# Kernel optimization log

Hardware: AMD Instinct MI355X
Metric: run time of the kernel (lower is better)

The kernel has to match this reference:

```python
import jax, jax.numpy as jnp
import numpy as np

DIM = 256
N_PATCHES = 2048
N_HEADS = 8
BATCH = 2


def setup_inputs() -> dict:
    key = jax.random.key(0)
    ks = jax.random.split(key, 8)
    d = DIM
    s = d ** -0.5
    return {
        "x": jax.random.normal(ks[0], (BATCH, N_PATCHES, d), dtype=jnp.float32),
        # weights stored (in_features, out_features) so y = x @ W + b
        "W_qk": jax.random.normal(ks[1], (d, 2 * d), dtype=jnp.float32) * s,
        "W_v": jax.random.normal(ks[2], (d, d), dtype=jnp.float32) * s,
        "W_proj": jax.random.normal(ks[3], (d, d), dtype=jnp.float32) * s,
        "b_proj": jnp.zeros((d,), dtype=jnp.float32),
        "W_pos": jax.random.normal(ks[4], (2, N_HEADS), dtype=jnp.float32) * 0.5,
        "b_pos": jnp.zeros((N_HEADS,), dtype=jnp.float32),
        "gating": jnp.ones((N_HEADS,), dtype=jnp.float32),
    }


def reference(x, W_qk, W_v, W_proj, b_proj, W_pos, b_pos, gating):
    B, N, C = x.shape
    H = gating.shape[0]
    Dh = C // H
    scale = Dh ** -0.5

    # content attention: q @ k^T softmax
    qk = (x @ W_qk).reshape(B, N, 2, H, Dh)
    q = jnp.transpose(qk[:, :, 0], (0, 2, 1, 3))  # [B,H,N,Dh]
    k = jnp.transpose(qk[:, :, 1], (0, 2, 1, 3))
    patch_score = jax.nn.softmax(jnp.einsum("bhnd,bhmd->bhnm", q, k) * scale, axis=-1)

    # positional attention from relative indices (d, |d|) -> per-head score
    idx = jnp.arange(N, dtype=jnp.float32)
    rel = idx[:, None] - idx[None, :]                      # [N,N]
    rel_feat = jnp.stack([rel, jnp.abs(rel)], axis=-1)     # [N,N,2]
    pos = rel_feat @ W_pos + b_pos                         # [N,N,H]
    pos_score = jax.nn.softmax(jnp.transpose(pos, (2, 0, 1)), axis=-1)  # [H,N,N]

    g = jax.nn.sigmoid(gating)[None, :, None, None]        # [1,H,1,1]
    attn = (1.0 - g) * patch_score + g * pos_score[None]   # [B,H,N,N]
    attn = attn / jnp.sum(attn, axis=-1, keepdims=True)

    v = jnp.transpose((x @ W_v).reshape(B, N, H, Dh), (0, 2, 1, 3))  # [B,H,N,Dh]
    out = jnp.einsum("bhnm,bhmd->bhnd", attn, v)
    out = jnp.transpose(out, (0, 2, 1, 3)).reshape(B, N, C)
    return out @ W_proj + b_proj
```

## Files before the change

### kernel.cpp

```cpp
#include <hip/hip_runtime.h>
#include <hip/hip_bf16.h>

#define DIM 256
#define NP 2048
#define NH 8
#define BATCH 2
#define DH 32

typedef __attribute__((ext_vector_type(8))) short bshort8;
typedef __attribute__((ext_vector_type(4))) short bshort4;
typedef __attribute__((ext_vector_type(4))) float f32x4;

#define LOG2E 1.44269504f
#define QSCALE (0.17677669529663687f * LOG2E)

union U16B { uint4 u; bshort8 s8; __hip_bfloat16 h[8]; };
union U8B  { uint2 u; bshort4 s4; __hip_bfloat16 h[4]; };

__device__ __forceinline__ float fexp2(float x) { return __builtin_amdgcn_exp2f(x); }
__device__ __forceinline__ unsigned packbf(float hi, float lo) {
    return __builtin_amdgcn_perm(__float_as_uint(hi), __float_as_uint(lo), 0x07060302u);
}

__device__ __forceinline__ int lds_addr(int row, int colg) {
    return row * 256 + (((colg ^ (row & 7)) & 31) << 3);
}

__global__ __launch_bounds__(256) void prep_kernel(
    const float* __restrict__ Wqk,
    const float* __restrict__ Wv,
    const float* __restrict__ Wproj,
    __hip_bfloat16* __restrict__ WT) {
    const int t = threadIdx.x;
    const int blk = blockIdx.x;
    __shared__ float ts[64][65];
    const int ct = blk >> 2, k0 = (blk & 3) * 64;
    const int c0 = ct * 64;
    const float* src; int ldw, cs0; float scl = 1.0f;
    if (ct < 8)       { src = Wqk;   ldw = 512; cs0 = c0;      if (ct < 4) scl = QSCALE; }
    else if (ct < 12) { src = Wv;    ldw = 256; cs0 = c0 - 512; }
    else              { src = Wproj; ldw = 256; cs0 = c0 - 768; }
    const int cc = t & 63, tq = t >> 6;
#pragma unroll
    for (int j = 0; j < 16; j++) {
        int kk = tq * 16 + j;
        ts[kk][cc] = src[(size_t)(k0 + kk) * ldw + cs0 + cc];
    }
    __syncthreads();
    const int kk2 = t & 63;
#pragma unroll
    for (int j = 0; j < 16; j++) {
        int cc2 = tq * 16 + j;
        WT[(size_t)(c0 + cc2) * 256 + k0 + kk2] = __float2bfloat16(ts[kk2][cc2] * scl);
    }
}

__global__ __launch_bounds__(256) void qkv_mfma(
    const float* __restrict__ x,
    const __hip_bfloat16* __restrict__ WT,
    __hip_bfloat16* __restrict__ q,
    __hip_bfloat16* __restrict__ k,
    __hip_bfloat16* __restrict__ vF) {
    __shared__ __align__(16) __hip_bfloat16 As[64 * 256];
    __shared__ __align__(16) __hip_bfloat16 Bs[64 * 256];
    const int t = threadIdx.x, lane = t & 63, wvid = t >> 6;
    const int l15 = lane & 15, l4 = lane >> 4;
    const int m0 = blockIdx.x * 64;
    const int nb0 = blockIdx.y * 64;

#pragma unroll
    for (int j = 0; j < 8; j++) {
        const int flat = j * 2048 + t * 8;
        const int row = flat >> 8, colg = (flat >> 3) & 31;
        float4 f0 = *(const float4*)(x + (size_t)m0 * 256 + flat);
        float4 f1 = *(const float4*)(x + (size_t)m0 * 256 + flat + 4);
        U16B a;
        a.h[0] = __float2bfloat16(f0.x); a.h[1] = __float2bfloat16(f0.y);
        a.h[2] = __float2bfloat16(f0.z); a.h[3] = __float2bfloat16(f0.w);
        a.h[4] = __float2bfloat16(f1.x); a.h[5] = __float2bfloat16(f1.y);
        a.h[6] = __float2bfloat16(f1.z); a.h[7] = __float2bfloat16(f1.w);
        *(uint4*)&As[lds_addr(row, colg)] = a.u;
        *(uint4*)&Bs[lds_addr(row, colg)] = *(const uint4*)(WT + (size_t)nb0 * 256 + flat);
    }
    __syncthreads();

    f32x4 acc[4] = {{0.f,0.f,0.f,0.f},{0.f,0.f,0.f,0.f},{0.f,0.f,0.f,0.f},{0.f,0.f,0.f,0.f}};
#pragma unroll
    for (int kk = 0; kk < 8; kk++) {
        const int colg = kk * 4 + l4;
        U16B bw; bw.u = *(const uint4*)&Bs[lds_addr(wvid * 16 + l15, colg)];
#pragma unroll
        for (int mt = 0; mt < 4; mt++) {
            U16B ax; ax.u = *(const uint4*)&As[lds_addr(mt * 16 + l15, colg)];
            acc[mt] = __builtin_amdgcn_mfma_f32_16x16x32_bf16(ax.s8, bw.s8, acc[mt], 0, 0, 0);
        }
    }

    if (nb0 < 512) {
        __syncthreads();
        __hip_bfloat16* Tr = As;
#pragma unroll
        for (int mt = 0; mt < 4; mt++)
#pragma unroll
            for (int r = 0; r < 4; r++)
                Tr[(mt * 16 + l4 * 4 + r) * 72 + wvid * 16 + l15] = __float2bfloat16(acc[mt][r]);
        __syncthreads();
        const int hh = t >> 7, row = (t >> 1) & 63, part = t & 1;
        const bool isq = (nb0 < 256);
        const int cc = (isq ? nb0 : nb0 - 256) + hh * 32;
        const int hOut = cc >> 5;
        const int tok = m0 + row;
        const int b = tok >> 11, n = tok & (NP - 1);
        __hip_bfloat16* dst = (isq ? q : k) + ((size_t)(b * NH + hOut) * NP + n) * DH + part * 16;
        uint4 w0 = *(const uint4*)&Tr[row * 72 + hh * 32 + part * 16];
        uint4 w1 = *(const uint4*)&Tr[row * 72 + hh * 32 + part * 16 + 8];
        *(uint4*)dst = w0;
        *(uint4*)(dst + 8) = w1;
    } else {
        const int cbase = (nb0 - 512) + wvid * 16;
        const int h = cbase >> 5;
        const int vh = (cbase >> 4) & 1;
        const int b = m0 >> 11;
#pragma unroll
        for (int mt = 0; mt < 4; mt++) {
            const int kt = ((m0 & (NP - 1)) >> 4) + mt;
            U8B vv;
#pragma unroll
            for (int r = 0; r < 4; r++) vv.h[r] = __float2bfloat16(acc[mt][r]);
            *(uint2*)(vF + ((((size_t)((b * NH + h) * 128 + kt)) * 2 + vh) * 64 + lane) * 4) = vv.u;
        }
    }
}

__global__ __launch_bounds__(512, 4) void attn_kernel(
    const __hip_bfloat16* __restrict__ qg,
    const __hip_bfloat16* __restrict__ kg,
    const __hip_bfloat16* __restrict__ vF,
    const float* __restrict__ Wpos,
    const float* __restrict__ bpos,
    const float* __restrict__ gating,
    __hip_bfloat16* __restrict__ ao) {
    __shared__ float cmb[4][2][32][16];
    __shared__ float cls[4][2][16];

    const int t = threadIdx.x;
    const int lane = t & 63, wvid = t >> 6;
    const int l15 = lane & 15, l4 = lane >> 4;
    const int qt = wvid & 3, kh = wvid >> 2;
    const int bh = blockIdx.x >> 5, qb = blockIdx.x & 31;
    const int h = bh & (NH - 1), b = bh >> 3;
    const int q0 = qb * 64 + qt * 16;
    const int myq = q0 + l15;

    const float w0 = Wpos[h] * LOG2E;
    const float w1 = Wpos[NH + h] * LOG2E;
    const float g = 1.0f / (1.0f + __expf(-gating[h]));
    const float nf = (float)myq;
    const float pmax = fmaxf(0.f, fmaxf((w0 + w1) * nf, (w1 - w0) * (2047.0f - nf)));
    const float npmax = -pmax;
    const float rA = fexp2(-(w0 + w1));
    const float rB = fexp2(w1 - w0);

    U16B qv;
    qv.u = *(const uint4*)(qg + ((size_t)bh * NP + myq) * DH + l4 * 8);

    const __hip_bfloat16* kbase = kg + (size_t)bh * NP * DH;
    const __hip_bfloat16* vbase = vF + (size_t)bh * 128 * 2 * 256;
    const int kstart = kh * 1024;

    f32x4 os0 = {0.f,0.f,0.f,0.f}, os1 = {0.f,0.f,0.f,0.f};
    f32x4 op0 = {0.f,0.f,0.f,0.f}, op1 = {0.f,0.f,0.f,0.f};
    float ls = 0.f, lp = 0.f;

#pragma unroll 2
    for (int it = 0; it < 16; ++it) {
        const int kb0 = kstart + it * 64;
        const int kt0 = kb0 >> 4;

        U8B vfr[8];
#pragma unroll
        for (int ktl = 0; ktl < 4; ktl++)
#pragma unroll
            for (int vh = 0; vh < 2; vh++)
                vfr[vh * 4 + ktl].u = *(const uint2*)(vbase +
                    (((size_t)(kt0 + ktl) * 2 + vh) * 64 + lane) * 4);
        U16B kf[4];
#pragma unroll
        for (int kt = 0; kt < 4; kt++)
            kf[kt].u = *(const uint4*)(kbase + (size_t)(kb0 + kt * 16 + l15) * DH + l4 * 8);

        f32x4 st4[4];
#pragma unroll
        for (int kt = 0; kt < 4; kt++)
            st4[kt] = __builtin_amdgcn_mfma_f32_16x16x32_bf16(
                kf[kt].s8, qv.s8, (f32x4){0.f,0.f,0.f,0.f}, 0, 0, 0);

#pragma unroll
        for (int kt = 0; kt < 4; kt++) {
            float es0 = fexp2(st4[kt][0]), es1 = fexp2(st4[kt][1]);
            float es2 = fexp2(st4[kt][2]), es3 = fexp2(st4[kt][3]);
            ls += (es0 + es1) + (es2 + es3);
            const float d0 = nf - (float)(kb0 + kt * 16 + l4 * 4);
            float ep0 = fexp2(fmaf(w1, fabsf(d0), fmaf(w0, d0, npmax)));
            float ep1 = ep0 * ((d0 >= 1.f) ? rA : rB);
            float ep2 = ep1 * ((d0 >= 2.f) ? rA : rB);
            float ep3 = ep2 * ((d0 >= 3.f) ? rA : rB);
            lp += (ep0 + ep1) + (ep2 + ep3);
            U8B pc, pp;
            pc.u.x = packbf(es1, es0); pc.u.y = packbf(es3, es2);
            pp.u.x = packbf(ep1, ep0); pp.u.y = packbf(ep3, ep2);
            os0 = __builtin_amdgcn_mfma_f32_16x16x16bf16_1k(vfr[kt].s4,     pc.s4, os0, 0, 0, 0);
            os1 = __builtin_amdgcn_mfma_f32_16x16x16bf16_1k(vfr[4 + kt].s4, pc.s4, os1, 0, 0, 0);
            op0 = __builtin_amdgcn_mfma_f32_16x16x16bf16_1k(vfr[kt].s4,     pp.s4, op0, 0, 0, 0);
            op1 = __builtin_amdgcn_mfma_f32_16x16x16bf16_1k(vfr[4 + kt].s4, pp.s4, op1, 0, 0, 0);
        }
    }

    ls += __shfl_xor(ls, 16, 64); ls += __shfl_xor(ls, 32, 64);
    lp += __shfl_xor(lp, 16, 64); lp += __shfl_xor(lp, 32, 64);

    if (kh == 1) {
#pragma unroll
        for (int r = 0; r < 4; r++) {
            cmb[qt][0][l4 * 4 + r][l15]      = os0[r];
            cmb[qt][0][16 + l4 * 4 + r][l15] = os1[r];
            cmb[qt][1][l4 * 4 + r][l15]      = op0[r];
            cmb[qt][1][16 + l4 * 4 + r][l15] = op1[r];
        }
        if (l4 == 0) { cls[qt][0][l15] = ls; cls[qt][1][l15] = lp; }
    }
    __syncthreads();
    if (kh == 0) {
        ls += cls[qt][0][l15]; lp += cls[qt][1][l15];
        const float cs = (1.0f - g) / ls;
        const float cp = g / lp;
        const size_t orow = ((size_t)b * NP + myq) * DIM + h * DH;
        U8B o0, o1;
#pragma unroll
        for (int r = 0; r < 4; r++) {
            o0.h[r] = __float2bfloat16(cs * (os0[r] + cmb[qt][0][l4 * 4 + r][l15]) +
                                       cp * (op0[r] + cmb[qt][1][l4 * 4 + r][l15]));
            o1.h[r] = __float2bfloat16(cs * (os1[r] + cmb[qt][0][16 + l4 * 4 + r][l15]) +
                                       cp * (op1[r] + cmb[qt][1][16 + l4 * 4 + r][l15]));
        }
        *(uint2*)(ao + orow + l4 * 4)      = o0.u;
        *(uint2*)(ao + orow + 16 + l4 * 4) = o1.u;
    }
}

__global__ __launch_bounds__(256) void proj_mfma(
    const __hip_bfloat16* __restrict__ ao,
    const __hip_bfloat16* __restrict__ WT,
    const float* __restrict__ bias,
    float* __restrict__ out) {
    __shared__ __align__(16) __hip_bfloat16 As[64 * 256];
    __shared__ __align__(16) __hip_bfloat16 Bs[64 * 256];
    const int t = threadIdx.x, lane = t & 63, wvid = t >> 6;
    const int l15 = lane & 15, l4 = lane >> 4;
    const int m0 = blockIdx.x * 64;
    const int nb0 = blockIdx.y * 64;
    const int nc = nb0 + wvid * 16 + l15;

#pragma unroll
    for (int j = 0; j < 8; j++) {
        const int flat = j * 2048 + t * 8;
        const int row = flat >> 8, colg = (flat >> 3) & 31;
        *(uint4*)&As[lds_addr(row, colg)] = *(const uint4*)(ao + (size_t)m0 * 256 + flat);
        *(uint4*)&Bs[lds_addr(row, colg)] = *(const uint4*)(WT + (size_t)(768 + nb0) * 256 + flat);
    }
    __syncthreads();

    f32x4 acc[4] = {{0.f,0.f,0.f,0.f},{0.f,0.f,0.f,0.f},{0.f,0.f,0.f,0.f},{0.f,0.f,0.f,0.f}};
#pragma unroll
    for (int kk = 0; kk < 8; kk++) {
        const int colg = kk * 4 + l4;
        U16B bw; bw.u = *(const uint4*)&Bs[lds_addr(wvid * 16 + l15, colg)];
#pragma unroll
        for (int mt = 0; mt < 4; mt++) {
            U16B ax; ax.u = *(const uint4*)&As[lds_addr(mt * 16 + l15, colg)];
            acc[mt] = __builtin_amdgcn_mfma_f32_16x16x32_bf16(ax.s8, bw.s8, acc[mt], 0, 0, 0);
        }
    }

    const float bb = bias[nc];
#pragma unroll
    for (int mt = 0; mt < 4; mt++)
#pragma unroll
        for (int r = 0; r < 4; r++) {
            int tok = m0 + mt * 16 + l4 * 4 + r;
            out[(size_t)tok * 256 + nc] = acc[mt][r] + bb;
        }
}

extern "C" void kernel_launch(void* const* d_in, const int* in_sizes, int n_in,
                              void* d_out, int out_size, void* d_ws, size_t ws_size,
                              hipStream_t stream) {
    const float* x      = (const float*)d_in[0];
    const float* Wqk    = (const float*)d_in[1];
    const float* Wv     = (const float*)d_in[2];
    const float* Wproj  = (const float*)d_in[3];
    const float* bproj  = (const float*)d_in[4];
    const float* Wpos   = (const float*)d_in[5];
    const float* bpos   = (const float*)d_in[6];
    const float* gating = (const float*)d_in[7];
    float* out = (float*)d_out;

    const size_t nElem = (size_t)BATCH * NP * DIM;
    char* w = (char*)d_ws;
    __hip_bfloat16* WT = (__hip_bfloat16*)w;
    __hip_bfloat16* q  = WT + 262144;
    __hip_bfloat16* k  = q + nElem;
    __hip_bfloat16* vF = k + nElem;
    __hip_bfloat16* ao = vF + nElem;

    prep_kernel<<<64, 256, 0, stream>>>(Wqk, Wv, Wproj, WT);
    qkv_mfma<<<dim3(64, 12), 256, 0, stream>>>(x, WT, q, k, vF);
    attn_kernel<<<BATCH * NH * (NP / 64), 512, 0, stream>>>(q, k, vF, Wpos, bpos, gating, ao);
    proj_mfma<<<dim3(64, 4), 256, 0, stream>>>(ao, WT, bproj, out);
}
```

Before: 115.9 us.

## Stage K/V tiles through double-buffered LDS and coalesce projection output stores

The attention kernel now loads each 64-key K and V tile cooperatively into double-buffered shared memory, prefetching the next tile into registers while computing on the current one. The four waves in a key half share one tile instead of each reloading it from global memory. A block barrier per iteration is added, and the unroll pragma is dropped. Separately, the projection kernel transposes its output through LDS so each thread writes contiguous float4s instead of scattered scalar stores.

```diff
diff --git a/kernel.cpp b/kernel.cpp
--- a/kernel.cpp
+++ b/kernel.cpp
@@ -140,6 +140,8 @@
     const float* __restrict__ bpos,
     const float* __restrict__ gating,
     __hip_bfloat16* __restrict__ ao) {
+    __shared__ __align__(16) __hip_bfloat16 Kt[2][2][64][40];
+    __shared__ __align__(16) __hip_bfloat16 Vf[2][2][2048];
     __shared__ float cmb[4][2][32][16];
     __shared__ float cls[4][2][16];
 
@@ -152,6 +154,16 @@
     const int q0 = qb * 64 + qt * 16;
     const int myq = q0 + l15;
 
+    const int st_ = t & 255;
+    const int kstart = kh * 1024;
+    const __hip_bfloat16* kptr = kg + (size_t)bh * NP * DH + (size_t)(kstart + (st_ >> 2)) * DH + (st_ & 3) * 8;
+    const __hip_bfloat16* vptr = vF + (size_t)bh * 65536 + (size_t)kstart * 32 + st_ * 8;
+
+    uint4 kreg = *(const uint4*)kptr;
+    uint4 vreg = *(const uint4*)vptr;
+    *(uint4*)&Kt[kh][0][st_ >> 2][(st_ & 3) * 8] = kreg;
+    *(uint4*)&Vf[kh][0][st_ * 8] = vreg;
+
     const float w0 = Wpos[h] * LOG2E;
     const float w1 = Wpos[NH + h] * LOG2E;
     const float g = 1.0f / (1.0f + __expf(-gating[h]));
@@ -164,37 +176,36 @@
     U16B qv;
     qv.u = *(const uint4*)(qg + ((size_t)bh * NP + myq) * DH + l4 * 8);
 
-    const __hip_bfloat16* kbase = kg + (size_t)bh * NP * DH;
-    const __hip_bfloat16* vbase = vF + (size_t)bh * 128 * 2 * 256;
-    const int kstart = kh * 1024;
+    __syncthreads();
 
     f32x4 os0 = {0.f,0.f,0.f,0.f}, os1 = {0.f,0.f,0.f,0.f};
     f32x4 op0 = {0.f,0.f,0.f,0.f}, op1 = {0.f,0.f,0.f,0.f};
     float ls = 0.f, lp = 0.f;
 
-#pragma unroll 2
     for (int it = 0; it < 16; ++it) {
+        const int cur = it & 1, nxt = cur ^ 1;
+
+        if (it < 15) {
+            kreg = *(const uint4*)(kptr + (size_t)(it + 1) * 64 * DH);
+            vreg = *(const uint4*)(vptr + (size_t)(it + 1) * 2048);
+        }
+
+        f32x4 st4[4];
+#pragma unroll
+        for (int kt = 0; kt < 4; kt++) {
+            U16B kf; kf.u = *(const uint4*)&Kt[kh][cur][kt * 16 + l15][l4 * 8];
+            st4[kt] = __builtin_amdgcn_mfma_f32_16x16x32_bf16(
+                kf.s8, qv.s8, (f32x4){0.f,0.f,0.f,0.f}, 0, 0, 0);
+        }
+
+        U8B vfr[8];
+#pragma unroll
+        for (int vh = 0; vh < 2; vh++)
+#pragma unroll
+            for (int ktl = 0; ktl < 4; ktl++)
+                vfr[vh * 4 + ktl].u = *(const uint2*)&Vf[kh][cur][((ktl * 2 + vh) * 64 + lane) * 4];
+
         const int kb0 = kstart + it * 64;
-        const int kt0 = kb0 >> 4;
-
-        U8B vfr[8];
-#pragma unroll
-        for (int ktl = 0; ktl < 4; ktl++)
-#pragma unroll
-            for (int vh = 0; vh < 2; vh++)
-                vfr[vh * 4 + ktl].u = *(const uint2*)(vbase +
-                    (((size_t)(kt0 + ktl) * 2 + vh) * 64 + lane) * 4);
-        U16B kf[4];
-#pragma unroll
-        for (int kt = 0; kt < 4; kt++)
-            kf[kt].u = *(const uint4*)(kbase + (size_t)(kb0 + kt * 16 + l15) * DH + l4 * 8);
-
-        f32x4 st4[4];
-#pragma unroll
-        for (int kt = 0; kt < 4; kt++)
-            st4[kt] = __builtin_amdgcn_mfma_f32_16x16x32_bf16(
-                kf[kt].s8, qv.s8, (f32x4){0.f,0.f,0.f,0.f}, 0, 0, 0);
-
 #pragma unroll
         for (int kt = 0; kt < 4; kt++) {
             float es0 = fexp2(st4[kt][0]), es1 = fexp2(st4[kt][1]);
@@ -214,6 +225,12 @@
             op0 = __builtin_amdgcn_mfma_f32_16x16x16bf16_1k(vfr[kt].s4,     pp.s4, op0, 0, 0, 0);
             op1 = __builtin_amdgcn_mfma_f32_16x16x16bf16_1k(vfr[4 + kt].s4, pp.s4, op1, 0, 0, 0);
         }
+
+        if (it < 15) {
+            *(uint4*)&Kt[kh][nxt][st_ >> 2][(st_ & 3) * 8] = kreg;
+            *(uint4*)&Vf[kh][nxt][st_ * 8] = vreg;
+        }
+        __syncthreads();
     }
 
     ls += __shfl_xor(ls, 16, 64); ls += __shfl_xor(ls, 32, 64);
@@ -283,13 +300,24 @@
     }
 
     const float bb = bias[nc];
+    __syncthreads();
+    float* Trf = (float*)As;
 #pragma unroll
     for (int mt = 0; mt < 4; mt++)
 #pragma unroll
-        for (int r = 0; r < 4; r++) {
-            int tok = m0 + mt * 16 + l4 * 4 + r;
-            out[(size_t)tok * 256 + nc] = acc[mt][r] + bb;
-        }
+        for (int r = 0; r < 4; r++)
+            Trf[(mt * 16 + l4 * 4 + r) * 68 + wvid * 16 + l15] = acc[mt][r] + bb;
+    __syncthreads();
+    const int row = t >> 2, seg = t & 3;
+    float4 v0 = *(const float4*)&Trf[row * 68 + seg * 16];
+    float4 v1 = *(const float4*)&Trf[row * 68 + seg * 16 + 4];
+    float4 v2 = *(const float4*)&Trf[row * 68 + seg * 16 + 8];
+    float4 v3 = *(const float4*)&Trf[row * 68 + seg * 16 + 12];
+    float* dst = out + (size_t)(m0 + row) * 256 + nb0 + seg * 16;
+    *(float4*)dst = v0;
+    *(float4*)(dst + 4) = v1;
+    *(float4*)(dst + 8) = v2;
+    *(float4*)(dst + 12) = v3;
 }
 
 extern "C" void kernel_launch(void* const* d_in, const int* in_sizes, int n_in,
```

New measurement: 109.1 us. 5.9% less time.
